# Kernel tuning notes

Measured on AMD Instinct MI355X. Metric: run time of the kernel, lower is better.

The kernel has to match this reference:

```python
import jax, jax.numpy as jnp
import numpy as np

TEMPERATURE = 0.5
EPS = 1e-8  # torch cosine_similarity norm clamp


def setup_inputs() -> dict:
    key = jax.random.key(0)
    k1, k2, k3 = jax.random.split(key, 3)
    N, D = 4096, 256
    z_i = jax.random.normal(k1, (N, D), dtype=jnp.float32)
    z_j = jax.random.normal(k2, (N, D), dtype=jnp.float32)
    weights = jax.random.uniform(k3, (N,), dtype=jnp.float32)
    return {"z_i": z_i, "z_j": z_j, "weights": weights}


def reference(z_i, z_j, weights):
    N = z_i.shape[0]
    z = jnp.concatenate([z_i, z_j], axis=0)  # [2N, D]
    # cosine similarity via normalized matmul (same math as broadcasted F.cosine_similarity)
    norm = jnp.maximum(jnp.linalg.norm(z, axis=1, keepdims=True), EPS)
    zn = z / norm
    sim = zn @ zn.T  # [2N, 2N]
    # positives: diagonals at offsets +N and -N
    sim_ij = jnp.diagonal(sim, offset=N)
    sim_ji = jnp.diagonal(sim, offset=-N)
    positives = jnp.concatenate([sim_ij, sim_ji], axis=0)  # [2N]
    mask = 1.0 - jnp.eye(2 * N, dtype=sim.dtype)
    denominator = jnp.sum(mask * jnp.exp(sim / TEMPERATURE), axis=1)  # [2N]
    numerator = jnp.exp(positives / TEMPERATURE)
    all_losses = -jnp.log(numerator / denominator)  # [2N]
    w2 = jnp.tile(weights, 2)  # weights.repeat(2)
    loss = jnp.sum(all_losses * w2) / jnp.sum(w2)
    return loss
```

## Files before the change

kernel.cpp:

```cpp
#include <hip/hip_runtime.h>
#include <hip/hip_bf16.h>

#define PN   4096
#define PN2  8192
#define PD   256
#define TILE 128
#define BK   64
#define NBLK (PN2 / TILE)
#define NTRI (NBLK * (NBLK + 1) / 2)

typedef __attribute__((ext_vector_type(8))) short bf16x8;
typedef __attribute__((ext_vector_type(4))) float f32x4;

typedef const __attribute__((address_space(1))) void* gas_ptr;
typedef __attribute__((address_space(3))) void* las_ptr;

__global__ __launch_bounds__(256) void normalize_kernel(
    const float* __restrict__ zi, const float* __restrict__ zj,
    __hip_bfloat16* __restrict__ zn, float* __restrict__ wlws,
    unsigned* __restrict__ ticket) {
  const int wave = threadIdx.x >> 6;
  const int lane = threadIdx.x & 63;
  const int r = blockIdx.x * 4 + wave;
  const float* src = (r < PN) ? (zi + (size_t)r * PD) : (zj + (size_t)(r - PN) * PD);
  float4 x = *(const float4*)(src + lane * 4);
  float s = x.x * x.x + x.y * x.y + x.z * x.z + x.w * x.w;
  #pragma unroll
  for (int off = 32; off >= 1; off >>= 1) s += __shfl_xor(s, off, 64);
  float inv = 1.0f / fmaxf(sqrtf(s), 1e-8f);
  union { ushort4 u; __hip_bfloat16 h[4]; } o;
  o.h[0] = __float2bfloat16(x.x * inv);
  o.h[1] = __float2bfloat16(x.y * inv);
  o.h[2] = __float2bfloat16(x.z * inv);
  o.h[3] = __float2bfloat16(x.w * inv);
  *(ushort4*)((unsigned short*)zn + (size_t)r * PD + lane * 4) = o.u;
  if (r == 0) {
    if (lane == 0) { wlws[0] = 0.0f; wlws[1] = 0.0f; }
    if (lane == 1) *ticket = 0u;
  }
}

__global__ __launch_bounds__(256) void simsum_kernel(
    const __hip_bfloat16* __restrict__ zn,
    float* __restrict__ rowpart, float* __restrict__ pos) {
  __shared__ char lds[2 * TILE * BK * 2];
  __shared__ float rowacc[TILE];
  __shared__ float colacc[TILE];
  char* As = lds;
  char* Bs = lds + TILE * BK * 2;

  const int tid  = threadIdx.x;
  if (tid < TILE) { rowacc[tid] = 0.0f; colacc[tid] = 0.0f; }

  const int idx = (int)((blockIdx.x & 7) * (NTRI / 8) + (blockIdx.x >> 3));
  int bj = (int)((sqrtf(8.0f * (float)idx + 1.0f) - 1.0f) * 0.5f);
  while ((bj + 1) * (bj + 2) / 2 <= idx) ++bj;
  while (bj * (bj + 1) / 2 > idx) --bj;
  const int bi = idx - bj * (bj + 1) / 2;
  const bool diagBlk = (bi == bj);
  const bool posBlk  = (bj == bi + PN / TILE);

  const int wave = tid >> 6;
  const int lane = tid & 63;
  const int quad = lane >> 4;
  const int c16  = lane & 15;
  const int rowBase = bi * TILE;
  const int colBase = bj * TILE;
  const int waveRow = (wave >> 1) * 64;
  const int waveCol = (wave & 1) * 64;

  f32x4 acc[4][4];
  #pragma unroll
  for (int i = 0; i < 4; ++i)
    #pragma unroll
    for (int j = 0; j < 4; ++j)
      acc[i][j] = (f32x4){0.f, 0.f, 0.f, 0.f};

  const int subrow = lane >> 3;
  const int slot   = lane & 7;
  const char* BsEff = diagBlk ? As : Bs;

  for (int kt = 0; kt < PD / BK; ++kt) {
    if (kt) __syncthreads();
    #pragma unroll
    for (int p = 0; p < 4; ++p) {
      int issue = wave * 4 + p;
      int r = issue * 8 + subrow;
      int c = slot ^ (r & 7);
      const __hip_bfloat16* ga = zn + (size_t)(rowBase + r) * PD + kt * BK + c * 8;
      __builtin_amdgcn_global_load_lds((gas_ptr)ga, (las_ptr)(As + issue * 1024), 16, 0, 0);
      if (!diagBlk) {
        const __hip_bfloat16* gb = zn + (size_t)(colBase + r) * PD + kt * BK + c * 8;
        __builtin_amdgcn_global_load_lds((gas_ptr)gb, (las_ptr)(Bs + issue * 1024), 16, 0, 0);
      }
    }
    __syncthreads();

    #pragma unroll
    for (int ki = 0; ki < 2; ++ki) {
      bf16x8 a[4], b[4];
      #pragma unroll
      for (int mi = 0; mi < 4; ++mi) {
        int r = waveRow + mi * 16 + c16;
        int ch = quad + ki * 4;
        a[mi] = *(const bf16x8*)(As + r * 128 + ((ch ^ (r & 7)) * 16));
      }
      #pragma unroll
      for (int ni = 0; ni < 4; ++ni) {
        int r = waveCol + ni * 16 + c16;
        int ch = quad + ki * 4;
        b[ni] = *(const bf16x8*)(BsEff + r * 128 + ((ch ^ (r & 7)) * 16));
      }
      #pragma unroll
      for (int mi = 0; mi < 4; ++mi)
        #pragma unroll
        for (int ni = 0; ni < 4; ++ni)
          acc[mi][ni] = __builtin_amdgcn_mfma_f32_16x16x32_bf16(a[mi], b[ni], acc[mi][ni], 0, 0, 0);
    }
  }

  float colsum[4] = {0.f, 0.f, 0.f, 0.f};
  #pragma unroll
  for (int mi = 0; mi < 4; ++mi) {
    int lrow = waveRow + mi * 16 + quad * 4;
    float rs[4] = {0.f, 0.f, 0.f, 0.f};
    #pragma unroll
    for (int ni = 0; ni < 4; ++ni) {
      int gcol = colBase + waveCol + ni * 16 + c16;
      #pragma unroll
      for (int t = 0; t < 4; ++t) {
        int grow = rowBase + lrow + t;
        float sim = acc[mi][ni][t];
        float e = __expf(2.0f * sim);
        if (diagBlk && gcol == grow) e = 0.0f;
        rs[t] += e;
        colsum[ni] += e;
        if (posBlk && gcol == grow + PN) {
          pos[grow] = sim;
          pos[grow + PN] = sim;
        }
      }
    }
    #pragma unroll
    for (int t = 0; t < 4; ++t) {
      #pragma unroll
      for (int off = 1; off <= 8; off <<= 1) rs[t] += __shfl_xor(rs[t], off, 64);
    }
    if (c16 == 0) {
      #pragma unroll
      for (int t = 0; t < 4; ++t) atomicAdd(&rowacc[lrow + t], rs[t]);
    }
  }
  if (!diagBlk) {
    #pragma unroll
    for (int ni = 0; ni < 4; ++ni) {
      float cs = colsum[ni];
      cs += __shfl_xor(cs, 16, 64);
      cs += __shfl_xor(cs, 32, 64);
      if (quad == 0) atomicAdd(&colacc[waveCol + ni * 16 + c16], cs);
    }
  }

  __syncthreads();
  if (tid < TILE) {
    rowpart[(size_t)bj * PN2 + rowBase + tid] = rowacc[tid];
    if (!diagBlk)
      rowpart[(size_t)bi * PN2 + colBase + tid] = colacc[tid];
  }
}

__global__ __launch_bounds__(256) void finalize_kernel(
    const float* __restrict__ rowpart, const float* __restrict__ pos,
    const float* __restrict__ w, float* __restrict__ wlws,
    unsigned* __restrict__ ticket, float* __restrict__ out) {
  const int tid = threadIdx.x;
  const int r = blockIdx.x * 256 + tid;
  float s = 0.0f;
  #pragma unroll 8
  for (int x = 0; x < NBLK; ++x) s += rowpart[(size_t)x * PN2 + r];
  float li = logf(s) - 2.0f * pos[r];
  float wi = w[r & (PN - 1)];
  float wl = wi * li, ws = wi;
  #pragma unroll
  for (int off = 32; off >= 1; off >>= 1) {
    wl += __shfl_xor(wl, off, 64);
    ws += __shfl_xor(ws, off, 64);
  }
  __shared__ float pl[4], pw[4];
  const int lane = tid & 63, wv = tid >> 6;
  if (lane == 0) { pl[wv] = wl; pw[wv] = ws; }
  __syncthreads();
  if (tid == 0) {
    atomicAdd(&wlws[0], pl[0] + pl[1] + pl[2] + pl[3]);
    atomicAdd(&wlws[1], pw[0] + pw[1] + pw[2] + pw[3]);
    __threadfence();
    if (atomicAdd(ticket, 1u) == 31) {
      float a = atomicAdd(&wlws[0], 0.0f);
      float b = atomicAdd(&wlws[1], 0.0f);
      out[0] = a / b;
    }
  }
}

extern "C" void kernel_launch(void* const* d_in, const int* in_sizes, int n_in,
                              void* d_out, int out_size, void* d_ws, size_t ws_size,
                              hipStream_t stream) {
  const float* zi = (const float*)d_in[0];
  const float* zj = (const float*)d_in[1];
  const float* w  = (const float*)d_in[2];
  float* out = (float*)d_out;

  __hip_bfloat16* zn = (__hip_bfloat16*)d_ws;
  float* rowpart = (float*)((char*)d_ws + (size_t)PN2 * PD * 2);
  float* pos     = rowpart + (size_t)NBLK * PN2;
  float* wlws    = pos + PN2;
  unsigned* ticket = (unsigned*)(wlws + 2);

  normalize_kernel<<<PN2 / 4, 256, 0, stream>>>(zi, zj, zn, wlws, ticket);
  simsum_kernel<<<NTRI, 256, 0, stream>>>(zn, rowpart, pos);
  finalize_kernel<<<32, 256, 0, stream>>>(rowpart, pos, w, wlws, ticket, out);
}
```

Measured before the change: 109.1 us.

## Enlarge similarity tiles to 256 with 512-thread blocks and double-buffered LDS loads

Doubles the output tile of the triangular similarity kernel to 256x256, using 8 waves per block, each computing a 128x64 sub-tile. The k-loop now double-buffers the direct global-to-LDS loads, so the next K slice is fetched while MFMAs run on the current one. The goals are more operand reuse per byte loaded, fewer partial row-sum slices for the finalize kernel to reduce, and overlap of load latency with compute. In exchange, the block needs 128KB of LDS and more accumulator registers, which likely limits residency to one block per CU. There are also only 528 large blocks, which risks poor load balance across the CUs.

```diff
diff --git a/kernel.cpp b/kernel.cpp
--- a/kernel.cpp
+++ b/kernel.cpp
@@ -4,7 +4,7 @@
 #define PN   4096
 #define PN2  8192
 #define PD   256
-#define TILE 128
+#define TILE 256
 #define BK   64
 #define NBLK (PN2 / TILE)
 #define NTRI (NBLK * (NBLK + 1) / 2)
@@ -40,14 +40,12 @@
   }
 }
 
-__global__ __launch_bounds__(256) void simsum_kernel(
+__global__ __launch_bounds__(512, 2) void simsum_kernel(
     const __hip_bfloat16* __restrict__ zn,
     float* __restrict__ rowpart, float* __restrict__ pos) {
-  __shared__ char lds[2 * TILE * BK * 2];
+  __shared__ char lds[2 * 2 * TILE * BK * 2];
   __shared__ float rowacc[TILE];
   __shared__ float colacc[TILE];
-  char* As = lds;
-  char* Bs = lds + TILE * BK * 2;
 
   const int tid  = threadIdx.x;
   if (tid < TILE) { rowacc[tid] = 0.0f; colacc[tid] = 0.0f; }
@@ -66,45 +64,48 @@
   const int c16  = lane & 15;
   const int rowBase = bi * TILE;
   const int colBase = bj * TILE;
-  const int waveRow = (wave >> 1) * 64;
-  const int waveCol = (wave & 1) * 64;
-
-  f32x4 acc[4][4];
-  #pragma unroll
-  for (int i = 0; i < 4; ++i)
+  const int waveRow = (wave >> 2) * 128;
+  const int waveCol = (wave & 3) * 64;
+  const int subrow = lane >> 3;
+  const int slot   = lane & 7;
+
+  f32x4 acc[8][4];
+  #pragma unroll
+  for (int i = 0; i < 8; ++i)
     #pragma unroll
     for (int j = 0; j < 4; ++j)
       acc[i][j] = (f32x4){0.f, 0.f, 0.f, 0.f};
 
-  const int subrow = lane >> 3;
-  const int slot   = lane & 7;
-  const char* BsEff = diagBlk ? As : Bs;
+#define STAGE(DSTA, DSTB, KT) do {                                            \
+    _Pragma("unroll")                                                         \
+    for (int p = 0; p < 4; ++p) {                                             \
+      int issue = wave * 4 + p;                      \
+      int rr = issue * 8 + subrow;                       \
+      int cc = slot ^ (rr & 7);                         \
+      const __hip_bfloat16* ga = zn + (size_t)(rowBase + rr) * PD + (KT) * BK + cc * 8; \
+      __builtin_amdgcn_global_load_lds((gas_ptr)ga, (las_ptr)((DSTA) + issue * 1024), 16, 0, 0); \
+      if (!diagBlk) {                                                         \
+        const __hip_bfloat16* gb = zn + (size_t)(colBase + rr) * PD + (KT) * BK + cc * 8; \
+        __builtin_amdgcn_global_load_lds((gas_ptr)gb, (las_ptr)((DSTB) + issue * 1024), 16, 0, 0); \
+      }                                                                       \
+    }                                                                         \
+  } while (0)
+
+  STAGE(lds, lds + 32768, 0);
+  __syncthreads();
 
   for (int kt = 0; kt < PD / BK; ++kt) {
-    if (kt) __syncthreads();
-    #pragma unroll
-    for (int p = 0; p < 4; ++p) {
-      int issue = wave * 4 + p;
-      int r = issue * 8 + subrow;
-      int c = slot ^ (r & 7);
-      const __hip_bfloat16* ga = zn + (size_t)(rowBase + r) * PD + kt * BK + c * 8;
-      __builtin_amdgcn_global_load_lds((gas_ptr)ga, (las_ptr)(As + issue * 1024), 16, 0, 0);
-      if (!diagBlk) {
-        const __hip_bfloat16* gb = zn + (size_t)(colBase + r) * PD + kt * BK + c * 8;
-        __builtin_amdgcn_global_load_lds((gas_ptr)gb, (las_ptr)(Bs + issue * 1024), 16, 0, 0);
-      }
-    }
-    __syncthreads();
+    char* As = lds + (kt & 1) * 65536;
+    char* Bs = As + 32768;
+    if (kt < PD / BK - 1) {
+      char* An = lds + ((kt + 1) & 1) * 65536;
+      STAGE(An, An + 32768, kt + 1);
+    }
+    const char* BsEff = diagBlk ? As : Bs;
 
     #pragma unroll
     for (int ki = 0; ki < 2; ++ki) {
-      bf16x8 a[4], b[4];
-      #pragma unroll
-      for (int mi = 0; mi < 4; ++mi) {
-        int r = waveRow + mi * 16 + c16;
-        int ch = quad + ki * 4;
-        a[mi] = *(const bf16x8*)(As + r * 128 + ((ch ^ (r & 7)) * 16));
-      }
+      bf16x8 b[4];
       #pragma unroll
       for (int ni = 0; ni < 4; ++ni) {
         int r = waveCol + ni * 16 + c16;
@@ -112,16 +113,22 @@
         b[ni] = *(const bf16x8*)(BsEff + r * 128 + ((ch ^ (r & 7)) * 16));
       }
       #pragma unroll
-      for (int mi = 0; mi < 4; ++mi)
+      for (int mi = 0; mi < 8; ++mi) {
+        int r = waveRow + mi * 16 + c16;
+        int ch = quad + ki * 4;
+        bf16x8 a = *(const bf16x8*)(As + r * 128 + ((ch ^ (r & 7)) * 16));
         #pragma unroll
         for (int ni = 0; ni < 4; ++ni)
-          acc[mi][ni] = __builtin_amdgcn_mfma_f32_16x16x32_bf16(a[mi], b[ni], acc[mi][ni], 0, 0, 0);
-    }
-  }
+          acc[mi][ni] = __builtin_amdgcn_mfma_f32_16x16x32_bf16(a, b[ni], acc[mi][ni], 0, 0, 0);
+      }
+    }
+    if (kt < PD / BK - 1) __syncthreads();
+  }
+#undef STAGE
 
   float colsum[4] = {0.f, 0.f, 0.f, 0.f};
   #pragma unroll
-  for (int mi = 0; mi < 4; ++mi) {
+  for (int mi = 0; mi < 8; ++mi) {
     int lrow = waveRow + mi * 16 + quad * 4;
     float rs[4] = {0.f, 0.f, 0.f, 0.f};
     #pragma unroll
@@ -176,7 +183,7 @@
   const int tid = threadIdx.x;
   const int r = blockIdx.x * 256 + tid;
   float s = 0.0f;
-  #pragma unroll 8
+  #pragma unroll
   for (int x = 0; x < NBLK; ++x) s += rowpart[(size_t)x * PN2 + r];
   float li = logf(s) - 2.0f * pos[r];
   float wi = w[r & (PN - 1)];
@@ -217,6 +224,6 @@
   unsigned* ticket = (unsigned*)(wlws + 2);
 
   normalize_kernel<<<PN2 / 4, 256, 0, stream>>>(zi, zj, zn, wlws, ticket);
-  simsum_kernel<<<NTRI, 256, 0, stream>>>(zn, rowpart, pos);
+  simsum_kernel<<<NTRI, 512, 0, stream>>>(zn, rowpart, pos);
   finalize_kernel<<<32, 256, 0, stream>>>(rowpart, pos, w, wlws, ticket, out);
 }
```

New measurement: 111.2 us. About the same (+1.9%).

## Switch similarity GEMM to FP8 MFMA and compute positives exactly in normalize

Applied to the files above, without the earlier changes.

The normalized embeddings are now quantized to FP8 E4M3 instead of bf16, and the tile GEMM uses the fp8 16x16x32 MFMA with BK=128. This halves operand bytes and halves the K-loop iterations. Positive-pair similarities are now computed in fp32 inside the normalize kernel, which handles z_i and z_j rows together, instead of being extracted from the GEMM epilogue. FP8 quantization adds error to the denominator sums, which may affect accuracy tolerance.

```diff
diff --git a/kernel.cpp b/kernel.cpp
--- a/kernel.cpp
+++ b/kernel.cpp
@@ -1,55 +1,70 @@
 #include <hip/hip_runtime.h>
 #include <hip/hip_bf16.h>
+#include <hip/hip_fp8.h>
 
 #define PN   4096
 #define PN2  8192
 #define PD   256
 #define TILE 128
-#define BK   64
+#define BK   128
 #define NBLK (PN2 / TILE)
 #define NTRI (NBLK * (NBLK + 1) / 2)
 
-typedef __attribute__((ext_vector_type(8))) short bf16x8;
 typedef __attribute__((ext_vector_type(4))) float f32x4;
-
 typedef const __attribute__((address_space(1))) void* gas_ptr;
 typedef __attribute__((address_space(3))) void* las_ptr;
 
 __global__ __launch_bounds__(256) void normalize_kernel(
     const float* __restrict__ zi, const float* __restrict__ zj,
-    __hip_bfloat16* __restrict__ zn, float* __restrict__ wlws,
-    unsigned* __restrict__ ticket) {
+    unsigned char* __restrict__ zn8, float* __restrict__ pos,
+    float* __restrict__ wlws, unsigned* __restrict__ ticket) {
   const int wave = threadIdx.x >> 6;
   const int lane = threadIdx.x & 63;
   const int r = blockIdx.x * 4 + wave;
-  const float* src = (r < PN) ? (zi + (size_t)r * PD) : (zj + (size_t)(r - PN) * PD);
-  float4 x = *(const float4*)(src + lane * 4);
-  float s = x.x * x.x + x.y * x.y + x.z * x.z + x.w * x.w;
-  #pragma unroll
-  for (int off = 32; off >= 1; off >>= 1) s += __shfl_xor(s, off, 64);
-  float inv = 1.0f / fmaxf(sqrtf(s), 1e-8f);
-  union { ushort4 u; __hip_bfloat16 h[4]; } o;
-  o.h[0] = __float2bfloat16(x.x * inv);
-  o.h[1] = __float2bfloat16(x.y * inv);
-  o.h[2] = __float2bfloat16(x.z * inv);
-  o.h[3] = __float2bfloat16(x.w * inv);
-  *(ushort4*)((unsigned short*)zn + (size_t)r * PD + lane * 4) = o.u;
-  if (r == 0) {
-    if (lane == 0) { wlws[0] = 0.0f; wlws[1] = 0.0f; }
-    if (lane == 1) *ticket = 0u;
+  float4 a = *(const float4*)(zi + (size_t)r * PD + lane * 4);
+  float4 b = *(const float4*)(zj + (size_t)r * PD + lane * 4);
+  float si = a.x * a.x + a.y * a.y + a.z * a.z + a.w * a.w;
+  float sj = b.x * b.x + b.y * b.y + b.z * b.z + b.w * b.w;
+  float d  = a.x * b.x + a.y * b.y + a.z * b.z + a.w * b.w;
+  #pragma unroll
+  for (int off = 32; off >= 1; off >>= 1) {
+    si += __shfl_xor(si, off, 64);
+    sj += __shfl_xor(sj, off, 64);
+    d  += __shfl_xor(d,  off, 64);
+  }
+  float ni = fmaxf(sqrtf(si), 1e-8f);
+  float nj = fmaxf(sqrtf(sj), 1e-8f);
+  if (lane == 0) {
+    float p = d / (ni * nj);
+    pos[r] = p;
+    pos[r + PN] = p;
+  }
+  float ia = 1.0f / ni, ib = 1.0f / nj;
+  union { unsigned u; unsigned char c[4]; } pa, pb;
+  pa.c[0] = __hip_cvt_float_to_fp8(a.x * ia, __HIP_SATFINITE, __HIP_E4M3);
+  pa.c[1] = __hip_cvt_float_to_fp8(a.y * ia, __HIP_SATFINITE, __HIP_E4M3);
+  pa.c[2] = __hip_cvt_float_to_fp8(a.z * ia, __HIP_SATFINITE, __HIP_E4M3);
+  pa.c[3] = __hip_cvt_float_to_fp8(a.w * ia, __HIP_SATFINITE, __HIP_E4M3);
+  pb.c[0] = __hip_cvt_float_to_fp8(b.x * ib, __HIP_SATFINITE, __HIP_E4M3);
+  pb.c[1] = __hip_cvt_float_to_fp8(b.y * ib, __HIP_SATFINITE, __HIP_E4M3);
+  pb.c[2] = __hip_cvt_float_to_fp8(b.z * ib, __HIP_SATFINITE, __HIP_E4M3);
+  pb.c[3] = __hip_cvt_float_to_fp8(b.w * ib, __HIP_SATFINITE, __HIP_E4M3);
+  *(unsigned*)(zn8 + (size_t)r * PD + lane * 4) = pa.u;
+  *(unsigned*)(zn8 + (size_t)(r + PN) * PD + lane * 4) = pb.u;
+  if (blockIdx.x == 0 && threadIdx.x == 0) {
+    wlws[0] = 0.0f; wlws[1] = 0.0f; *ticket = 0u;
   }
 }
 
 __global__ __launch_bounds__(256) void simsum_kernel(
-    const __hip_bfloat16* __restrict__ zn,
-    float* __restrict__ rowpart, float* __restrict__ pos) {
-  __shared__ char lds[2 * TILE * BK * 2];
+    const unsigned char* __restrict__ zn8, float* __restrict__ rowpart) {
+  __shared__ char lds[2 * TILE * BK];
   __shared__ float rowacc[TILE];
   __shared__ float colacc[TILE];
   char* As = lds;
-  char* Bs = lds + TILE * BK * 2;
-
-  const int tid  = threadIdx.x;
+  char* Bs = lds + TILE * BK;
+
+  const int tid = threadIdx.x;
   if (tid < TILE) { rowacc[tid] = 0.0f; colacc[tid] = 0.0f; }
 
   const int idx = (int)((blockIdx.x & 7) * (NTRI / 8) + (blockIdx.x >> 3));
@@ -58,7 +73,6 @@
   while (bj * (bj + 1) / 2 > idx) --bj;
   const int bi = idx - bj * (bj + 1) / 2;
   const bool diagBlk = (bi == bj);
-  const bool posBlk  = (bj == bi + PN / TILE);
 
   const int wave = tid >> 6;
   const int lane = tid & 63;
@@ -68,6 +82,8 @@
   const int colBase = bj * TILE;
   const int waveRow = (wave >> 1) * 64;
   const int waveCol = (wave & 1) * 64;
+  const int subrow = lane >> 3;
+  const int slot   = lane & 7;
 
   f32x4 acc[4][4];
   #pragma unroll
@@ -76,8 +92,6 @@
     for (int j = 0; j < 4; ++j)
       acc[i][j] = (f32x4){0.f, 0.f, 0.f, 0.f};
 
-  const int subrow = lane >> 3;
-  const int slot   = lane & 7;
   const char* BsEff = diagBlk ? As : Bs;
 
   for (int kt = 0; kt < PD / BK; ++kt) {
@@ -85,37 +99,37 @@
     #pragma unroll
     for (int p = 0; p < 4; ++p) {
       int issue = wave * 4 + p;
-      int r = issue * 8 + subrow;
-      int c = slot ^ (r & 7);
-      const __hip_bfloat16* ga = zn + (size_t)(rowBase + r) * PD + kt * BK + c * 8;
+      int rr = issue * 8 + subrow;
+      int cc = slot ^ (rr & 7);
+      const unsigned char* ga = zn8 + (size_t)(rowBase + rr) * PD + kt * BK + cc * 16;
       __builtin_amdgcn_global_load_lds((gas_ptr)ga, (las_ptr)(As + issue * 1024), 16, 0, 0);
       if (!diagBlk) {
-        const __hip_bfloat16* gb = zn + (size_t)(colBase + r) * PD + kt * BK + c * 8;
+        const unsigned char* gb = zn8 + (size_t)(colBase + rr) * PD + kt * BK + cc * 16;
         __builtin_amdgcn_global_load_lds((gas_ptr)gb, (las_ptr)(Bs + issue * 1024), 16, 0, 0);
       }
     }
     __syncthreads();
 
     #pragma unroll
-    for (int ki = 0; ki < 2; ++ki) {
-      bf16x8 a[4], b[4];
+    for (int ki = 0; ki < 4; ++ki) {
+      const int G  = ki * 2 + (quad >> 1);
+      const int h8 = (quad & 1) * 8;
+      long a[4], b[4];
       #pragma unroll
       for (int mi = 0; mi < 4; ++mi) {
         int r = waveRow + mi * 16 + c16;
-        int ch = quad + ki * 4;
-        a[mi] = *(const bf16x8*)(As + r * 128 + ((ch ^ (r & 7)) * 16));
+        a[mi] = *(const long*)(As + r * 128 + (((G ^ (r & 7)) << 4) + h8));
       }
       #pragma unroll
       for (int ni = 0; ni < 4; ++ni) {
         int r = waveCol + ni * 16 + c16;
-        int ch = quad + ki * 4;
-        b[ni] = *(const bf16x8*)(BsEff + r * 128 + ((ch ^ (r & 7)) * 16));
+        b[ni] = *(const long*)(BsEff + r * 128 + (((G ^ (r & 7)) << 4) + h8));
       }
       #pragma unroll
       for (int mi = 0; mi < 4; ++mi)
         #pragma unroll
         for (int ni = 0; ni < 4; ++ni)
-          acc[mi][ni] = __builtin_amdgcn_mfma_f32_16x16x32_bf16(a[mi], b[ni], acc[mi][ni], 0, 0, 0);
+          acc[mi][ni] = __builtin_amdgcn_mfma_f32_16x16x32_fp8_fp8(a[mi], b[ni], acc[mi][ni], 0, 0, 0);
     }
   }
 
@@ -130,15 +144,10 @@
       #pragma unroll
       for (int t = 0; t < 4; ++t) {
         int grow = rowBase + lrow + t;
-        float sim = acc[mi][ni][t];
-        float e = __expf(2.0f * sim);
+        float e = __expf(2.0f * acc[mi][ni][t]);
         if (diagBlk && gcol == grow) e = 0.0f;
         rs[t] += e;
         colsum[ni] += e;
-        if (posBlk && gcol == grow + PN) {
-          pos[grow] = sim;
-          pos[grow + PN] = sim;
-        }
       }
     }
     #pragma unroll
@@ -176,7 +185,7 @@
   const int tid = threadIdx.x;
   const int r = blockIdx.x * 256 + tid;
   float s = 0.0f;
-  #pragma unroll 8
+  #pragma unroll
   for (int x = 0; x < NBLK; ++x) s += rowpart[(size_t)x * PN2 + r];
   float li = logf(s) - 2.0f * pos[r];
   float wi = w[r & (PN - 1)];
@@ -210,13 +219,13 @@
   const float* w  = (const float*)d_in[2];
   float* out = (float*)d_out;
 
-  __hip_bfloat16* zn = (__hip_bfloat16*)d_ws;
-  float* rowpart = (float*)((char*)d_ws + (size_t)PN2 * PD * 2);
+  unsigned char* zn8 = (unsigned char*)d_ws;
+  float* rowpart = (float*)((char*)d_ws + (size_t)PN2 * PD);
   float* pos     = rowpart + (size_t)NBLK * PN2;
   float* wlws    = pos + PN2;
   unsigned* ticket = (unsigned*)(wlws + 2);
 
-  normalize_kernel<<<PN2 / 4, 256, 0, stream>>>(zi, zj, zn, wlws, ticket);
-  simsum_kernel<<<NTRI, 256, 0, stream>>>(zn, rowpart, pos);
+  normalize_kernel<<<PN / 4, 256, 0, stream>>>(zi, zj, zn8, pos, wlws, ticket);
+  simsum_kernel<<<NTRI, 256, 0, stream>>>(zn8, rowpart);
   finalize_kernel<<<32, 256, 0, stream>>>(rowpart, pos, w, wlws, ticket, out);
 }
```

Measured after the change: 112.5 us. +3.0%, slower.
